# Kernel optimization log

Measured on AMD Instinct MI355X. Metric: run time of the kernel, lower is better.

## Reference

```python
import jax, jax.numpy as jnp
import numpy as np

N_NODES = 50000
N_EDGES = 600000
IN_DIM, HID, OUT_DIM = 128, 128, 64


def setup_inputs() -> dict:
    key = jax.random.key(0)
    ks = jax.random.split(key, 12)
    h = jax.random.normal(ks[0], (N_NODES, IN_DIM), dtype=jnp.float32)
    src = jax.random.randint(ks[1], (N_EDGES,), 0, N_NODES, dtype=jnp.int32)
    dst = jax.random.randint(ks[2], (N_EDGES,), 0, N_NODES, dtype=jnp.int32)
    dims = [(IN_DIM, HID), (HID, HID), (HID, HID), (HID, OUT_DIM)]
    params = {}
    for i, (di, do) in enumerate(dims):
        scale = 1.0 / np.sqrt(di)
        params[f"W{i}"] = jax.random.uniform(ks[3 + i], (di, do), jnp.float32, -scale, scale)
        params[f"b{i}"] = jnp.zeros((do,), jnp.float32)
    return dict(h=h, src=src, dst=dst, **params)


def _gcn_layer(h, W, b, src, dst, norm_src, norm_dst, n_nodes):
    # DGL GraphConv, norm='both': D^{-1/2} A D^{-1/2} (h W) + b
    x = (h * norm_src) @ W              # [N, out]
    agg = jax.ops.segment_sum(x[src], dst, num_segments=n_nodes)
    return agg * norm_dst + b


def reference(h, src, dst, W0, b0, W1, b1, W2, b2, W3, b3):
    n = h.shape[0]
    ones = jnp.ones((src.shape[0],), h.dtype)
    deg_out = jnp.clip(jax.ops.segment_sum(ones, src, num_segments=n), 1.0)
    deg_in = jnp.clip(jax.ops.segment_sum(ones, dst, num_segments=n), 1.0)
    norm_src = (deg_out ** -0.5)[:, None]
    norm_dst = (deg_in ** -0.5)[:, None]
    Ws = [(W0, b0), (W1, b1), (W2, b2), (W3, b3)]
    for i, (W, b) in enumerate(Ws):
        h = _gcn_layer(h, W, b, src, dst, norm_src, norm_dst, n)
        if i != len(Ws) - 1:
            h = jax.nn.relu(h)  # dropout is identity in eval mode
    return h
```

## Files before the change

### kernel.cpp

```cpp
#include <hip/hip_runtime.h>


namespace {

constexpr int NN = 50000;
constexpr int NE = 600000;
constexpr int SCAN_BLK = 256;
constexpr int NBLK = (NN + SCAN_BLK - 1) / SCAN_BLK;
constexpr int DEG_BLOCKS = 256;
constexpr int GEMM_TILES = (NN + 63) / 64;

typedef unsigned short bhalf;

__device__ inline float blo(unsigned int v) {
  return __uint_as_float(v << 16);
}
__device__ inline float bhi(unsigned int v) {
  return __uint_as_float(v & 0xFFFF0000u);
}
__device__ inline unsigned int f2b_bits(float f) {
  unsigned int b = __float_as_uint(f);
  return b + 0x7FFFu + ((b >> 16) & 1u);
}
__device__ inline unsigned int pack2(float lo, float hi) {
  return (f2b_bits(lo) >> 16) | (f2b_bits(hi) & 0xFFFF0000u);
}

__global__ __launch_bounds__(SCAN_BLK) void scan1_norm(const int* __restrict__ dego,
                                                       const int* __restrict__ degi,
                                                       int* __restrict__ bsum,
                                                       float* __restrict__ ns,
                                                       float* __restrict__ nd) {
  __shared__ int ws[SCAN_BLK / 64];
  int i = blockIdx.x * SCAN_BLK + threadIdx.x;
  int v = 0;
  if (i < NN) {
    int din = degi[i];
    int dout = dego[i];
    v = din;
    int a = dout < 1 ? 1 : dout;
    int b = din < 1 ? 1 : din;
    ns[i] = 1.0f / sqrtf((float)a);
    nd[i] = 1.0f / sqrtf((float)b);
  }
#pragma unroll
  for (int off = 32; off; off >>= 1) v += __shfl_down(v, off, 64);
  int lane = threadIdx.x & 63, w = threadIdx.x >> 6;
  if (lane == 0) ws[w] = v;
  __syncthreads();
  if (threadIdx.x == 0) {
    int s = 0;
#pragma unroll
    for (int k = 0; k < SCAN_BLK / 64; ++k) s += ws[k];
    bsum[blockIdx.x] = s;
  }
}

__global__ __launch_bounds__(256) void scan_phase2(const int* __restrict__ bsum,
                                                   int* __restrict__ bpre,
                                                   int* __restrict__ rowptr) {
  __shared__ int s[256];
  int t = threadIdx.x;
  int v = (t < NBLK) ? bsum[t] : 0;
  s[t] = v;
  __syncthreads();
  for (int off = 1; off < 256; off <<= 1) {
    int u = (t >= off) ? s[t - off] : 0;
    __syncthreads();
    s[t] += u;
    __syncthreads();
  }
  if (t < NBLK) bpre[t] = s[t] - v;
  if (t == 255) rowptr[NN] = s[255];
}

__global__ __launch_bounds__(SCAN_BLK) void scan_phase3(const int* __restrict__ deg,
                                                        const int* __restrict__ bpre,
                                                        int* __restrict__ rowptr) {
  __shared__ int s[SCAN_BLK];
  int t = threadIdx.x;
  int i = blockIdx.x * SCAN_BLK + t;
  int v = (i < NN) ? deg[i] : 0;
  s[t] = v;
  __syncthreads();
  for (int off = 1; off < SCAN_BLK; off <<= 1) {
    int u = (t >= off) ? s[t - off] : 0;
    __syncthreads();
    s[t] += u;
    __syncthreads();
  }
  if (i < NN) rowptr[i] = bpre[blockIdx.x] + s[t] - v;
}

__global__ void scatter_kernel(const int* __restrict__ src, const int* __restrict__ dst,
                               const int* __restrict__ le, const int* __restrict__ rowptr,
                               int* __restrict__ col) {
  int e = blockIdx.x * blockDim.x + threadIdx.x;
  if (e < NE) col[rowptr[dst[e]] + le[e]] = src[e];
}

template <int DO, bool USE_NS, typename TH>
__device__ void gemm_body(const TH* __restrict__ h, const float* __restrict__ W,
                          const float* __restrict__ ns, bhalf* __restrict__ x,
                          int row0, float* hs, float* wl) {
  constexpr int CH = DO / 64;
  const int tid = threadIdx.x;

  if constexpr (sizeof(TH) == 4) {
#pragma unroll
    for (int it = 0; it < 8; ++it) {
      int flat = it * 256 + tid;
      int row = flat >> 5;
      int c = flat & 31;
      int grow = row0 + row;
      float4 hv = make_float4(0.f, 0.f, 0.f, 0.f);
      float sc = 0.f;
      if (grow < NN) {
        hv = *reinterpret_cast<const float4*>(&h[(size_t)grow * 128 + c * 4]);
        sc = USE_NS ? ns[grow] : 1.0f;
      }
      float* d = &hs[row * 132 + c * 4];
      d[0] = hv.x * sc; d[1] = hv.y * sc; d[2] = hv.z * sc; d[3] = hv.w * sc;
    }
  } else {
#pragma unroll
    for (int it = 0; it < 4; ++it) {
      int flat = it * 256 + tid;
      int row = flat >> 4;
      int c8 = (flat & 15) * 8;
      int grow = row0 + row;
      uint4 v = make_uint4(0u, 0u, 0u, 0u);
      float sc = 0.f;
      if (grow < NN) {
        v = *reinterpret_cast<const uint4*>(&h[(size_t)grow * 128 + c8]);
        sc = USE_NS ? ns[grow] : 1.0f;
      }
      float* d = &hs[row * 132 + c8];
      d[0] = blo(v.x) * sc; d[1] = bhi(v.x) * sc;
      d[2] = blo(v.y) * sc; d[3] = bhi(v.y) * sc;
      d[4] = blo(v.z) * sc; d[5] = bhi(v.z) * sc;
      d[6] = blo(v.w) * sc; d[7] = bhi(v.w) * sc;
    }
  }

  const int rq = tid >> 4;
  const int cq = tid & 15;

  for (int ch = 0; ch < CH; ++ch) {
    __syncthreads();
#pragma unroll
    for (int it = 0; it < 8; ++it) {
      int flat = it * 256 + tid;
      int k = flat >> 4;
      int c4 = flat & 15;
      *reinterpret_cast<float4*>(&wl[k * 64 + c4 * 4]) =
          *reinterpret_cast<const float4*>(&W[k * DO + ch * 64 + c4 * 4]);
    }
    __syncthreads();

    float acc[4][4] = {{0.f}};
#pragma unroll 4
    for (int k4 = 0; k4 < 32; ++k4) {
      float hv[4][4], wv[4][4];
#pragma unroll
      for (int i = 0; i < 4; ++i) {
        float4 t = *reinterpret_cast<const float4*>(&hs[(rq * 4 + i) * 132 + k4 * 4]);
        hv[i][0] = t.x; hv[i][1] = t.y; hv[i][2] = t.z; hv[i][3] = t.w;
      }
#pragma unroll
      for (int kk = 0; kk < 4; ++kk) {
        float4 t = *reinterpret_cast<const float4*>(&wl[(k4 * 4 + kk) * 64 + cq * 4]);
        wv[kk][0] = t.x; wv[kk][1] = t.y; wv[kk][2] = t.z; wv[kk][3] = t.w;
      }
#pragma unroll
      for (int i = 0; i < 4; ++i)
#pragma unroll
        for (int kk = 0; kk < 4; ++kk)
#pragma unroll
          for (int j = 0; j < 4; ++j)
            acc[i][j] = fmaf(hv[i][kk], wv[kk][j], acc[i][j]);
    }

#pragma unroll
    for (int i = 0; i < 4; ++i) {
      int row = row0 + rq * 4 + i;
      if (row < NN) {
        uint2 p;
        p.x = pack2(acc[i][0], acc[i][1]);
        p.y = pack2(acc[i][2], acc[i][3]);
        *reinterpret_cast<uint2*>(&x[(size_t)row * DO + ch * 64 + cq * 4]) = p;
      }
    }
  }
}

__global__ __launch_bounds__(256, 2) void gemm0_deg_kernel(
    const float* __restrict__ h, const float* __restrict__ W,
    bhalf* __restrict__ x,
    const int* __restrict__ src, const int* __restrict__ dst,
    int* __restrict__ dego, int* __restrict__ degi, int* __restrict__ le) {
  __shared__ __align__(16) float hs[64 * 132];
  __shared__ __align__(16) float wl[128 * 64];
  if (blockIdx.x < DEG_BLOCKS) {
    const int stride = DEG_BLOCKS * 256;
    for (int e = blockIdx.x * 256 + threadIdx.x; e < NE; e += stride) {
      atomicAdd(&dego[src[e]], 1);
      le[e] = atomicAdd(&degi[dst[e]], 1);
    }
    return;
  }
  gemm_body<128, false, float>(h, W, nullptr, x, (blockIdx.x - DEG_BLOCKS) * 64, hs, wl);
}

template <int DO>
__global__ __launch_bounds__(256, 2) void gemm_ns(const bhalf* __restrict__ h,
                                                  const float* __restrict__ W,
                                                  const float* __restrict__ ns,
                                                  bhalf* __restrict__ x) {
  __shared__ __align__(16) float hs[64 * 132];
  __shared__ __align__(16) float wl[128 * 64];
  gemm_body<DO, true, bhalf>(h, W, ns, x, blockIdx.x * 64, hs, wl);
}

template <int D, bool RELU, bool NSRC, bool OUTBF>
__global__ __launch_bounds__(256) void gather_kernel(const bhalf* __restrict__ x,
                                                     const int* __restrict__ rowptr,
                                                     const int* __restrict__ col,
                                                     const float* __restrict__ nd,
                                                     const float* __restrict__ b,
                                                     const float* __restrict__ nsv,
                                                     void* __restrict__ outp) {
  constexpr int LPR = D / 8;
  constexpr int EPW = 64 / LPR;
  const int wid = (blockIdx.x * blockDim.x + threadIdx.x) >> 6;
  const int lane = threadIdx.x & 63;
  if (wid >= NN) return;
  const int sub = lane / LPR;
  const int ci = (lane % LPR) * 8;
  const int beg = rowptr[wid];
  const int end = rowptr[wid + 1];

  float a[8];
#pragma unroll
  for (int k = 0; k < 8; ++k) a[k] = 0.f;

  int e = beg + sub;
  for (; e + EPW < end; e += 2 * EPW) {
    int c0 = col[e];
    int c1 = col[e + EPW];
    float s0 = NSRC ? nsv[c0] : 1.0f;
    float s1 = NSRC ? nsv[c1] : 1.0f;
    uint4 v0 = *reinterpret_cast<const uint4*>(&x[(size_t)c0 * D + ci]);
    uint4 v1 = *reinterpret_cast<const uint4*>(&x[(size_t)c1 * D + ci]);
    float f0[8], f1[8];
    f0[0] = blo(v0.x); f0[1] = bhi(v0.x); f0[2] = blo(v0.y); f0[3] = bhi(v0.y);
    f0[4] = blo(v0.z); f0[5] = bhi(v0.z); f0[6] = blo(v0.w); f0[7] = bhi(v0.w);
    f1[0] = blo(v1.x); f1[1] = bhi(v1.x); f1[2] = blo(v1.y); f1[3] = bhi(v1.y);
    f1[4] = blo(v1.z); f1[5] = bhi(v1.z); f1[6] = blo(v1.w); f1[7] = bhi(v1.w);
    if (NSRC) {
#pragma unroll
      for (int k = 0; k < 8; ++k) a[k] = fmaf(s0, f0[k], fmaf(s1, f1[k], a[k]));
    } else {
#pragma unroll
      for (int k = 0; k < 8; ++k) a[k] += f0[k] + f1[k];
    }
  }
  if (e < end) {
    int c0 = col[e];
    float s0 = NSRC ? nsv[c0] : 1.0f;
    uint4 v0 = *reinterpret_cast<const uint4*>(&x[(size_t)c0 * D + ci]);
    float f0[8];
    f0[0] = blo(v0.x); f0[1] = bhi(v0.x); f0[2] = blo(v0.y); f0[3] = bhi(v0.y);
    f0[4] = blo(v0.z); f0[5] = bhi(v0.z); f0[6] = blo(v0.w); f0[7] = bhi(v0.w);
    if (NSRC) {
#pragma unroll
      for (int k = 0; k < 8; ++k) a[k] = fmaf(s0, f0[k], a[k]);
    } else {
#pragma unroll
      for (int k = 0; k < 8; ++k) a[k] += f0[k];
    }
  }

#pragma unroll
  for (int off = LPR; off < 64; off <<= 1) {
#pragma unroll
    for (int k = 0; k < 8; ++k) a[k] += __shfl_xor(a[k], off, 64);
  }

  if (lane < LPR) {
    const float s = nd[wid];
    float4 b0 = *reinterpret_cast<const float4*>(&b[ci]);
    float4 b1 = *reinterpret_cast<const float4*>(&b[ci + 4]);
    float r[8];
    r[0] = fmaf(a[0], s, b0.x); r[1] = fmaf(a[1], s, b0.y);
    r[2] = fmaf(a[2], s, b0.z); r[3] = fmaf(a[3], s, b0.w);
    r[4] = fmaf(a[4], s, b1.x); r[5] = fmaf(a[5], s, b1.y);
    r[6] = fmaf(a[6], s, b1.z); r[7] = fmaf(a[7], s, b1.w);
    if (RELU) {
#pragma unroll
      for (int k = 0; k < 8; ++k) r[k] = fmaxf(r[k], 0.f);
    }
    if constexpr (OUTBF) {
      bhalf* out = (bhalf*)outp;
      uint4 p;
      p.x = pack2(r[0], r[1]);
      p.y = pack2(r[2], r[3]);
      p.z = pack2(r[4], r[5]);
      p.w = pack2(r[6], r[7]);
      *reinterpret_cast<uint4*>(&out[(size_t)wid * D + ci]) = p;
    } else {
      float* out = (float*)outp;
      *reinterpret_cast<float4*>(&out[(size_t)wid * D + ci]) =
          make_float4(r[0], r[1], r[2], r[3]);
      *reinterpret_cast<float4*>(&out[(size_t)wid * D + ci + 4]) =
          make_float4(r[4], r[5], r[6], r[7]);
    }
  }
}

}

extern "C" void kernel_launch(void* const* d_in, const int* in_sizes, int n_in,
                              void* d_out, int out_size, void* d_ws, size_t ws_size,
                              hipStream_t stream) {
  const float* h0  = (const float*)d_in[0];
  const int*   src = (const int*)d_in[1];
  const int*   dst = (const int*)d_in[2];
  const float* W0 = (const float*)d_in[3];
  const float* b0 = (const float*)d_in[4];
  const float* W1 = (const float*)d_in[5];
  const float* b1 = (const float*)d_in[6];
  const float* W2 = (const float*)d_in[7];
  const float* b2 = (const float*)d_in[8];
  const float* W3 = (const float*)d_in[9];
  const float* b3 = (const float*)d_in[10];
  float* out = (float*)d_out;

  char* w = (char*)d_ws;
  size_t off = 0;
  auto take = [&](size_t bytes) {
    char* p = w + off;
    off = (off + bytes + 255) & ~size_t(255);
    return p;
  };
  int*   deg_out = (int*)take(NN * 4);
  int*   deg_in  = (int*)take(NN * 4);
  float* nsrc    = (float*)take(NN * 4);
  float* ndst    = (float*)take(NN * 4);
  int*   rowptr  = (int*)take((NN + 1) * 4);
  int*   le      = (int*)take(NE * 4);
  int*   col     = (int*)take(NE * 4);
  int*   bsum    = (int*)take(NBLK * 4);
  int*   bpre    = (int*)take(NBLK * 4);
  bhalf* xbuf    = (bhalf*)take((size_t)NN * 128 * 2);
  bhalf* hbuf    = (bhalf*)take((size_t)NN * 128 * 2);
  (void)ws_size; (void)in_sizes; (void)n_in; (void)out_size;

  hipMemsetAsync(deg_out, 0, (size_t)((char*)nsrc - (char*)deg_out), stream);

  const int EB = (NE + 255) / 256;

  gemm0_deg_kernel<<<DEG_BLOCKS + GEMM_TILES, 256, 0, stream>>>(
      h0, W0, xbuf, src, dst, deg_out, deg_in, le);
  scan1_norm<<<NBLK, SCAN_BLK, 0, stream>>>(deg_out, deg_in, bsum, nsrc, ndst);
  scan_phase2<<<1, 256, 0, stream>>>(bsum, bpre, rowptr);
  scan_phase3<<<NBLK, SCAN_BLK, 0, stream>>>(deg_in, bpre, rowptr);
  scatter_kernel<<<EB, 256, 0, stream>>>(src, dst, le, rowptr, col);

  const int GATHER_BLOCKS = (NN * 64 + 255) / 256;

  gather_kernel<128, true, true, true><<<GATHER_BLOCKS, 256, 0, stream>>>(
      xbuf, rowptr, col, ndst, b0, nsrc, hbuf);
  gemm_ns<128><<<GEMM_TILES, 256, 0, stream>>>(hbuf, W1, nsrc, xbuf);
  gather_kernel<128, true, false, true><<<GATHER_BLOCKS, 256, 0, stream>>>(
      xbuf, rowptr, col, ndst, b1, nullptr, hbuf);
  gemm_ns<128><<<GEMM_TILES, 256, 0, stream>>>(hbuf, W2, nsrc, xbuf);
  gather_kernel<128, true, false, true><<<GATHER_BLOCKS, 256, 0, stream>>>(
      xbuf, rowptr, col, ndst, b2, nullptr, hbuf);
  gemm_ns<64><<<GEMM_TILES, 256, 0, stream>>>(hbuf, W3, nsrc, xbuf);
  gather_kernel<64, false, false, false><<<GATHER_BLOCKS, 256, 0, stream>>>(
      xbuf, rowptr, col, ndst, b3, nullptr, out);
}
```

Baseline: 302.3 us.

## Use bf16 MFMA for hidden-layer GEMMs with pre-transposed bf16 weights

Replaces the FP32 LDS-tiled SIMT GEMM for layers 1-3 with a per-wave 16-row tile that runs the bf16 MFMA 16x16x32 instruction, reading activations and weights straight from global memory. Weights are transposed and converted to bf16 inside the scan kernel launch. The norm_src scaling now happens after the matmul rather than before, and weights are rounded to bf16, which adds a little precision loss. The GEMM now relies on NN being a multiple of 16 and writes outputs as scalar bf16 stores.

```diff
diff --git a/kernel.cpp b/kernel.cpp
--- a/kernel.cpp
+++ b/kernel.cpp
@@ -9,8 +9,12 @@
 constexpr int NBLK = (NN + SCAN_BLK - 1) / SCAN_BLK;
 constexpr int DEG_BLOCKS = 256;
 constexpr int GEMM_TILES = (NN + 63) / 64;
+constexpr int WCVT_ELEMS = 128 * 128 + 128 * 128 + 128 * 64;
+constexpr int WCVT_BLOCKS = WCVT_ELEMS / 256;
 
 typedef unsigned short bhalf;
+typedef __attribute__((ext_vector_type(8))) short short8v;
+typedef __attribute__((ext_vector_type(4))) float f32x4;
 
 __device__ inline float blo(unsigned int v) {
   return __uint_as_float(v << 16);
@@ -25,12 +29,30 @@
 __device__ inline unsigned int pack2(float lo, float hi) {
   return (f2b_bits(lo) >> 16) | (f2b_bits(hi) & 0xFFFF0000u);
 }
-
-__global__ __launch_bounds__(SCAN_BLK) void scan1_norm(const int* __restrict__ dego,
-                                                       const int* __restrict__ degi,
-                                                       int* __restrict__ bsum,
-                                                       float* __restrict__ ns,
-                                                       float* __restrict__ nd) {
+__device__ inline bhalf f2b(float f) { return (bhalf)(f2b_bits(f) >> 16); }
+
+__global__ __launch_bounds__(SCAN_BLK) void scan1_norm_wcvt(
+    const int* __restrict__ dego, const int* __restrict__ degi,
+    int* __restrict__ bsum, float* __restrict__ ns, float* __restrict__ nd,
+    const float* __restrict__ W1, const float* __restrict__ W2,
+    const float* __restrict__ W3, bhalf* __restrict__ wt1,
+    bhalf* __restrict__ wt2, bhalf* __restrict__ wt3) {
+  if (blockIdx.x >= NBLK) {
+    int flat = (blockIdx.x - NBLK) * 256 + threadIdx.x;
+    if (flat < 16384) {
+      int j = flat >> 7, k = flat & 127;
+      wt1[flat] = f2b(W1[k * 128 + j]);
+    } else if (flat < 32768) {
+      int f = flat - 16384;
+      int j = f >> 7, k = f & 127;
+      wt2[f] = f2b(W2[k * 128 + j]);
+    } else {
+      int f = flat - 32768;
+      int j = f >> 7, k = f & 127;
+      wt3[f] = f2b(W3[k * 64 + j]);
+    }
+    return;
+  }
   __shared__ int ws[SCAN_BLK / 64];
   int i = blockIdx.x * SCAN_BLK + threadIdx.x;
   int v = 0;
@@ -99,54 +121,26 @@
   if (e < NE) col[rowptr[dst[e]] + le[e]] = src[e];
 }
 
-template <int DO, bool USE_NS, typename TH>
-__device__ void gemm_body(const TH* __restrict__ h, const float* __restrict__ W,
-                          const float* __restrict__ ns, bhalf* __restrict__ x,
-                          int row0, float* hs, float* wl) {
-  constexpr int CH = DO / 64;
+__device__ void gemm0_body(const float* __restrict__ h, const float* __restrict__ W,
+                           bhalf* __restrict__ x, int row0, float* hs, float* wl) {
   const int tid = threadIdx.x;
-
-  if constexpr (sizeof(TH) == 4) {
-#pragma unroll
-    for (int it = 0; it < 8; ++it) {
-      int flat = it * 256 + tid;
-      int row = flat >> 5;
-      int c = flat & 31;
-      int grow = row0 + row;
-      float4 hv = make_float4(0.f, 0.f, 0.f, 0.f);
-      float sc = 0.f;
-      if (grow < NN) {
-        hv = *reinterpret_cast<const float4*>(&h[(size_t)grow * 128 + c * 4]);
-        sc = USE_NS ? ns[grow] : 1.0f;
-      }
-      float* d = &hs[row * 132 + c * 4];
-      d[0] = hv.x * sc; d[1] = hv.y * sc; d[2] = hv.z * sc; d[3] = hv.w * sc;
-    }
-  } else {
-#pragma unroll
-    for (int it = 0; it < 4; ++it) {
-      int flat = it * 256 + tid;
-      int row = flat >> 4;
-      int c8 = (flat & 15) * 8;
-      int grow = row0 + row;
-      uint4 v = make_uint4(0u, 0u, 0u, 0u);
-      float sc = 0.f;
-      if (grow < NN) {
-        v = *reinterpret_cast<const uint4*>(&h[(size_t)grow * 128 + c8]);
-        sc = USE_NS ? ns[grow] : 1.0f;
-      }
-      float* d = &hs[row * 132 + c8];
-      d[0] = blo(v.x) * sc; d[1] = bhi(v.x) * sc;
-      d[2] = blo(v.y) * sc; d[3] = bhi(v.y) * sc;
-      d[4] = blo(v.z) * sc; d[5] = bhi(v.z) * sc;
-      d[6] = blo(v.w) * sc; d[7] = bhi(v.w) * sc;
-    }
+#pragma unroll
+  for (int it = 0; it < 8; ++it) {
+    int flat = it * 256 + tid;
+    int row = flat >> 5;
+    int c = flat & 31;
+    int grow = row0 + row;
+    float4 hv = make_float4(0.f, 0.f, 0.f, 0.f);
+    if (grow < NN)
+      hv = *reinterpret_cast<const float4*>(&h[(size_t)grow * 128 + c * 4]);
+    float* d = &hs[row * 132 + c * 4];
+    d[0] = hv.x; d[1] = hv.y; d[2] = hv.z; d[3] = hv.w;
   }
 
   const int rq = tid >> 4;
   const int cq = tid & 15;
 
-  for (int ch = 0; ch < CH; ++ch) {
+  for (int ch = 0; ch < 2; ++ch) {
     __syncthreads();
 #pragma unroll
     for (int it = 0; it < 8; ++it) {
@@ -154,7 +148,7 @@
       int k = flat >> 4;
       int c4 = flat & 15;
       *reinterpret_cast<float4*>(&wl[k * 64 + c4 * 4]) =
-          *reinterpret_cast<const float4*>(&W[k * DO + ch * 64 + c4 * 4]);
+          *reinterpret_cast<const float4*>(&W[k * 128 + ch * 64 + c4 * 4]);
     }
     __syncthreads();
 
@@ -188,7 +182,7 @@
         uint2 p;
         p.x = pack2(acc[i][0], acc[i][1]);
         p.y = pack2(acc[i][2], acc[i][3]);
-        *reinterpret_cast<uint2*>(&x[(size_t)row * DO + ch * 64 + cq * 4]) = p;
+        *reinterpret_cast<uint2*>(&x[(size_t)row * 128 + ch * 64 + cq * 4]) = p;
       }
     }
   }
@@ -209,17 +203,51 @@
     }
     return;
   }
-  gemm_body<128, false, float>(h, W, nullptr, x, (blockIdx.x - DEG_BLOCKS) * 64, hs, wl);
+  gemm0_body(h, W, x, (blockIdx.x - DEG_BLOCKS) * 64, hs, wl);
 }
 
 template <int DO>
-__global__ __launch_bounds__(256, 2) void gemm_ns(const bhalf* __restrict__ h,
-                                                  const float* __restrict__ W,
-                                                  const float* __restrict__ ns,
-                                                  bhalf* __restrict__ x) {
-  __shared__ __align__(16) float hs[64 * 132];
-  __shared__ __align__(16) float wl[128 * 64];
-  gemm_body<DO, true, bhalf>(h, W, ns, x, blockIdx.x * 64, hs, wl);
+__global__ __launch_bounds__(256, 2) void gemm_mfma(const bhalf* __restrict__ h,
+                                                    const bhalf* __restrict__ wt,
+                                                    const float* __restrict__ ns,
+                                                    bhalf* __restrict__ x) {
+  constexpr int CF = DO / 16;
+  const int lane = threadIdx.x & 63;
+  const int wv = threadIdx.x >> 6;
+  const int tile = blockIdx.x * 4 + wv;
+  if (tile >= NN / 16) return;
+  const int row0 = tile * 16;
+  const size_t arow = (size_t)(row0 + (lane & 15)) * 128;
+  const int koff = (lane >> 4) * 8;
+  const int bcol = lane & 15;
+
+  f32x4 acc[CF];
+#pragma unroll
+  for (int cf = 0; cf < CF; ++cf) acc[cf] = (f32x4){0.f, 0.f, 0.f, 0.f};
+
+#pragma unroll
+  for (int ks = 0; ks < 4; ++ks) {
+    const int k0 = ks * 32 + koff;
+    short8v av = *reinterpret_cast<const short8v*>(&h[arow + k0]);
+#pragma unroll
+    for (int cf = 0; cf < CF; ++cf) {
+      short8v bv = *reinterpret_cast<const short8v*>(
+          &wt[(size_t)(cf * 16 + bcol) * 128 + k0]);
+      acc[cf] = __builtin_amdgcn_mfma_f32_16x16x32_bf16(av, bv, acc[cf], 0, 0, 0);
+    }
+  }
+
+  const int crow = row0 + ((lane >> 4) << 2);
+  float nsv[4];
+#pragma unroll
+  for (int r = 0; r < 4; ++r) nsv[r] = ns[crow + r];
+#pragma unroll
+  for (int cf = 0; cf < CF; ++cf) {
+#pragma unroll
+    for (int r = 0; r < 4; ++r) {
+      x[(size_t)(crow + r) * DO + cf * 16 + bcol] = f2b(acc[cf][r] * nsv[r]);
+    }
+  }
 }
 
 template <int D, bool RELU, bool NSRC, bool OUTBF>
@@ -354,6 +382,9 @@
   int*   bpre    = (int*)take(NBLK * 4);
   bhalf* xbuf    = (bhalf*)take((size_t)NN * 128 * 2);
   bhalf* hbuf    = (bhalf*)take((size_t)NN * 128 * 2);
+  bhalf* wt1     = (bhalf*)take(128 * 128 * 2);
+  bhalf* wt2     = (bhalf*)take(128 * 128 * 2);
+  bhalf* wt3     = (bhalf*)take(64 * 128 * 2);
   (void)ws_size; (void)in_sizes; (void)n_in; (void)out_size;
 
   hipMemsetAsync(deg_out, 0, (size_t)((char*)nsrc - (char*)deg_out), stream);
@@ -362,22 +393,24 @@
 
   gemm0_deg_kernel<<<DEG_BLOCKS + GEMM_TILES, 256, 0, stream>>>(
       h0, W0, xbuf, src, dst, deg_out, deg_in, le);
-  scan1_norm<<<NBLK, SCAN_BLK, 0, stream>>>(deg_out, deg_in, bsum, nsrc, ndst);
+  scan1_norm_wcvt<<<NBLK + WCVT_BLOCKS, SCAN_BLK, 0, stream>>>(
+      deg_out, deg_in, bsum, nsrc, ndst, W1, W2, W3, wt1, wt2, wt3);
   scan_phase2<<<1, 256, 0, stream>>>(bsum, bpre, rowptr);
   scan_phase3<<<NBLK, SCAN_BLK, 0, stream>>>(deg_in, bpre, rowptr);
   scatter_kernel<<<EB, 256, 0, stream>>>(src, dst, le, rowptr, col);
 
   const int GATHER_BLOCKS = (NN * 64 + 255) / 256;
+  const int MFMA_BLOCKS = (NN / 16 + 3) / 4;
 
   gather_kernel<128, true, true, true><<<GATHER_BLOCKS, 256, 0, stream>>>(
       xbuf, rowptr, col, ndst, b0, nsrc, hbuf);
-  gemm_ns<128><<<GEMM_TILES, 256, 0, stream>>>(hbuf, W1, nsrc, xbuf);
+  gemm_mfma<128><<<MFMA_BLOCKS, 256, 0, stream>>>(hbuf, wt1, nsrc, xbuf);
   gather_kernel<128, true, false, true><<<GATHER_BLOCKS, 256, 0, stream>>>(
       xbuf, rowptr, col, ndst, b1, nullptr, hbuf);
-  gemm_ns<128><<<GEMM_TILES, 256, 0, stream>>>(hbuf, W2, nsrc, xbuf);
+  gemm_mfma<128><<<MFMA_BLOCKS, 256, 0, stream>>>(hbuf, wt2, nsrc, xbuf);
   gather_kernel<128, true, false, true><<<GATHER_BLOCKS, 256, 0, stream>>>(
       xbuf, rowptr, col, ndst, b2, nullptr, hbuf);
-  gemm_ns<64><<<GEMM_TILES, 256, 0, stream>>>(hbuf, W3, nsrc, xbuf);
+  gemm_mfma<64><<<MFMA_BLOCKS, 256, 0, stream>>>(hbuf, wt3, nsrc, xbuf);
   gather_kernel<64, false, false, false><<<GATHER_BLOCKS, 256, 0, stream>>>(
       xbuf, rowptr, col, ndst, b3, nullptr, out);
 }
```

Result: faster. 266.1 us (-12.0%).
